# Optimization experiments

Hardware: AMD Instinct MI355X
Metric: run time of the kernel (lower is better)

Reference implementation:

```python
import jax, jax.numpy as jnp
import numpy as np

MAX_IT = 10
LAMBDA_ROF = 4.0
SIGMA = 1.0 / (7.0 * 0.01)
TAU = 0.01
THETA = 0.5
M, N = 2048, 2048


def forward_grad(x):
    """x: [1,M,N] -> [2,M,N]; forward differences, zero at last col/row."""
    gh = jnp.pad(x[0, :, 1:] - x[0, :, :-1], ((0, 0), (0, 1)))  # horizontal
    gv = jnp.pad(x[0, 1:, :] - x[0, :-1, :], ((0, 1), (0, 0)))  # vertical
    return jnp.stack([gh, gv], axis=0)


def backward_div(y):
    """y: [2,M,N] -> [1,M,N]; adjoint backward-difference divergence."""
    yh, yv = y[0], y[1]
    d_h = jnp.concatenate([yh[:, :1], yh[:, 1:-1] - yh[:, :-2], -yh[:, -2:-1]], axis=1)
    d_v = jnp.concatenate([yv[:1, :], yv[1:-1, :] - yv[:-2, :], -yv[-2:-1, :]], axis=0)
    return (d_h + d_v)[None]  # [1,M,N]


def prox_linf_ball(p, r):
    # Torch original builds m1/m2 from p.data (no grad flow) -> stop_gradient.
    m1 = jnp.maximum(p - r, 0.0)
    m2 = jnp.maximum(-p - r, 0.0)
    return p - jax.lax.stop_gradient(m1 - m2)  # == clamp(p, -r, r) in value


def setup_inputs() -> dict:
    key = jax.random.key(0)
    k1, k2 = jax.random.split(key)
    img_obs = jax.random.uniform(k1, (1, M, N), dtype=jnp.float32)
    w1 = jnp.array([0.5], dtype=jnp.float32)  # nn.Parameter [1]
    w2 = jnp.array([0.4], dtype=jnp.float32)  # nn.Parameter [1]
    return {"img_obs": img_obs, "w1": w1, "w2": w2}


def reference(img_obs, w1, w2):
    x = img_obs
    x_tilde = img_obs
    y = forward_grad(x)  # [2,M,N]
    # w_term built from y.data in torch -> constant wrt autodiff
    w_term = jax.lax.stop_gradient(jnp.exp(-jnp.abs(y)))
    w = w1[0] + w2[0] * w_term  # [2,M,N]
    for _ in range(MAX_IT):
        # dual weighted update + L-inf prox
        y = y + SIGMA * w * forward_grad(x_tilde)
        y = prox_linf_ball(y, 1.0)
        # primal weighted update (ROF)
        x_old = x
        x = (x + TAU * backward_div(w * y) + LAMBDA_ROF * TAU * img_obs) / (1.0 + LAMBDA_ROF * TAU)
        # primal over-relaxation
        x_tilde = x + THETA * (x - x_old)
    return x_tilde
```

## Files before the change

### kernel.cpp

```cpp
#include <hip/hip_runtime.h>


namespace {
constexpr int M = 2048, N = 2048;
constexpr float SIGMA     = 1.0f / (7.0f * 0.01f);
constexpr float TAU       = 0.01f;
constexpr float TAUIS     = TAU * (7.0f * 0.01f);
constexpr float LT        = 4.0f * 0.01f;
constexpr float INV_DEN   = 1.0f / (1.0f + 4.0f * 0.01f);
constexpr int TW = 64, TH = 48;
constexpr int PC = 88;
constexpr int PR = 68;
constexpr int UPR = 22;
constexpr int PROC = 67;
constexpr int NU = PROC * UPR;
constexpr int NT = 512;
constexpr int NPASS = 3;
constexpr int GY = (M + TH - 1) / TH;
}

typedef _Float16 h4 __attribute__((ext_vector_type(4)));

__device__ inline h4 h4splat(float v) {
    _Float16 s = (_Float16)v;
    return (h4){s, s, s, s};
}
__device__ inline int imax(int a, int b) { return a > b ? a : b; }

__global__ __launch_bounds__(NT, 4) void pd_fused(
    const float* __restrict__ img, float* __restrict__ out,
    const float* __restrict__ w1p, const float* __restrict__ w2p)
{
    __shared__ __align__(16) float    sXT[PR * PC];
    __shared__ __align__(16) _Float16 sQV[PR * PC];
    __shared__ __align__(16) _Float16 sQH3[1536];

    const int tid  = threadIdx.x;
    const int lane = tid & 63;
    const int c0 = blockIdx.x * TW, r0 = blockIdx.y * TH;
    const int gr0 = r0 - 10, gc0 = c0 - 12;
    const float w1 = w1p[0], w2 = w2p[0];

    int bF_[NPASS], dth_[NPASS];
    #pragma unroll
    for (int p = 0; p < NPASS; ++p) {
        int u = tid + p * NT;
        int li = u / UPR, uj = u - li * UPR;
        int lc = uj * 4;
        bF_[p] = u * 4;
        int d = imax(imax(9 - li, li - (TH + 9)), imax(8 - lc, lc - 75));
        d = imax(d, 0);
        if (u >= NU) d = 100;
        dth_[p] = d;
    }

    #pragma unroll
    for (int p = 0; p < NPASS; ++p) {
        int su = tid + p * NT;
        if (su < PR * UPR) {
            int li = su / UPR, uj = su - li * UPR;
            int gi = gr0 + li, gj = gc0 + uj * 4;
            float4 v = make_float4(0.f, 0.f, 0.f, 0.f);
            if ((unsigned)gi < (unsigned)M && (unsigned)gj <= (unsigned)(N - 4))
                v = *(const float4*)&img[(size_t)gi * N + gj];
            *(float4*)&sXT[su * 4] = v;
        }
    }
    __syncthreads();

    float xr[NPASS][4], xt[NPASS][4];
    h4 xi[NPASS], yh[NPASS], yv[NPASS], swh[NPASS], swv[NPASS], qH[NPASS];

    #pragma unroll
    for (int p = 0; p < NPASS; ++p) {
        int u = tid + p * NT, bF = bF_[p];
        float4 c = make_float4(0.f, 0.f, 0.f, 0.f);
        if (u < NU) c = *(const float4*)&sXT[bF];
        float rr = __shfl_down(c.x, 1, 64);
        if (u < NU) {
            int li = u / UPR;
            int gi = gr0 + li, gjb = gc0 + (u - li * UPR) * 4;
            if (lane == 63) rr = sXT[bF + 4];
            float4 dn = *(const float4*)&sXT[bF + PC];
            float ca[4] = {c.x, c.y, c.z, c.w};
            float da[4] = {dn.x, dn.y, dn.z, dn.w};
            bool rok = (unsigned)gi < (unsigned)M;
            bool vok = rok && (gi < M - 1);
            h4 qv;
            #pragma unroll
            for (int l = 0; l < 4; ++l) {
                int gj = gjb + l;
                bool cok = (unsigned)gj < (unsigned)N;
                bool hok = rok && cok && (gj < N - 1);
                bool vk  = vok && cok;
                float nxt = (l < 3) ? ca[l + 1] : rr;
                float gh = hok ? nxt - ca[l] : 0.f;
                float gv = vk  ? da[l] - ca[l] : 0.f;
                float wh = fmaf(w2, __expf(-fabsf(gh)), w1);
                float wv = fmaf(w2, __expf(-fabsf(gv)), w1);
                float y0h = fminf(fmaxf(gh * fmaf(SIGMA, wh, 1.f), -1.f), 1.f);
                float y0v = fminf(fmaxf(gv * fmaf(SIGMA, wv, 1.f), -1.f), 1.f);
                float sh = hok ? SIGMA * wh : 0.f;
                float sv = vk  ? SIGMA * wv : 0.f;
                yh[p][l]  = (_Float16)y0h;  yv[p][l]  = (_Float16)y0v;
                swh[p][l] = (_Float16)sh;   swv[p][l] = (_Float16)sv;
                qH[p][l]  = (_Float16)(sh * y0h);
                qv[l]     = (_Float16)(sv * y0v);
                xr[p][l] = ca[l]; xt[p][l] = ca[l];
                xi[p][l] = (_Float16)ca[l];
            }
            *(h4*)&sQV[bF] = qv;
            sQH3[u] = qH[p][3];
        }
    }
    __syncthreads();

    auto dual = [&](int rem) {
        #pragma unroll
        for (int p = 0; p < NPASS; ++p) {
            float rr = __shfl_down(xt[p][0], 1, 64);
            if (rem >= dth_[p]) {
                int bF = bF_[p];
                if (lane == 63) rr = sXT[bF + 4];
                float4 dn = *(const float4*)&sXT[bF + PC];
                float da[4] = {dn.x, dn.y, dn.z, dn.w};
                h4 ghh, gvh;
                #pragma unroll
                for (int l = 0; l < 4; ++l) {
                    float nxt = (l < 3) ? xt[p][l + 1] : rr;
                    ghh[l] = (_Float16)(nxt - xt[p][l]);
                    gvh[l] = (_Float16)(da[l] - xt[p][l]);
                }
                h4 nh = yh[p] + swh[p] * ghh;
                h4 nv = yv[p] + swv[p] * gvh;
                nh = __builtin_elementwise_min(__builtin_elementwise_max(nh, h4splat(-1.f)), h4splat(1.f));
                nv = __builtin_elementwise_min(__builtin_elementwise_max(nv, h4splat(-1.f)), h4splat(1.f));
                yh[p] = nh; yv[p] = nv;
                h4 qh = swh[p] * nh;
                h4 qv = swv[p] * nv;
                qH[p] = qh;
                *(h4*)&sQV[bF] = qv;
                sQH3[bF >> 2] = qh[3];
            }
        }
    };

    auto primal = [&](int rem) {
        #pragma unroll
        for (int p = 0; p < NPASS; ++p) {
            if (rem >= dth_[p]) {
                int bF = bF_[p];
                int bu = (bF >= UPR * 4) ? bF - PC : bF;
                h4 qvu = *(const h4*)&sQV[bu];
                h4 qv  = *(const h4*)&sQV[bF];
                _Float16 qhl = sQH3[imax((bF >> 2) - 1, 0)];
                h4 qsh;
                qsh[0] = qhl; qsh[1] = qH[p][0]; qsh[2] = qH[p][1]; qsh[3] = qH[p][2];
                h4 dvg = (qH[p] - qsh) + (qv - qvu);
                float xtv[4];
                #pragma unroll
                for (int l = 0; l < 4; ++l) {
                    float dv = (float)dvg[l];
                    float xo = xr[p][l];
                    float xn = (fmaf(TAUIS, dv, xo) + LT * (float)xi[p][l]) * INV_DEN;
                    xr[p][l] = xn;
                    float v = fmaf(0.5f, xn - xo, xn);
                    xt[p][l] = v; xtv[l] = v;
                }
                *(float4*)&sXT[bF] = make_float4(xtv[0], xtv[1], xtv[2], xtv[3]);
            }
        }
    };

    primal(9);
    __syncthreads();
    #pragma unroll 1
    for (int t = 1; t < 10; ++t) {
        int rem = 9 - t;
        dual(rem);
        __syncthreads();
        primal(rem);
        __syncthreads();
    }

    #pragma unroll
    for (int v = tid; v < TH * (TW / 4); v += NT) {
        int row = v >> 4;
        int cu  = v & 15;
        int gi = r0 + row;
        if (gi < M) {
            float4 o = *(const float4*)&sXT[(10 + row) * PC + 12 + 4 * cu];
            *(float4*)&out[(size_t)gi * N + (c0 + 4 * cu)] = o;
        }
    }
}

extern "C" void kernel_launch(void* const* d_in, const int* in_sizes, int n_in,
                              void* d_out, int out_size, void* d_ws, size_t ws_size,
                              hipStream_t stream)
{
    const float* img = (const float*)d_in[0];
    const float* w1  = (const float*)d_in[1];
    const float* w2  = (const float*)d_in[2];
    float* out = (float*)d_out;

    dim3 grid(N / TW, GY);
    pd_fused<<<grid, NT, 0, stream>>>(img, out, w1, w2);
}
```

Before: 121.9 us.

## Store over-relaxed primal tile in fp16 shared memory and write output directly

```diff
diff --git a/kernel.cpp b/kernel.cpp
--- a/kernel.cpp
+++ b/kernel.cpp
@@ -4,8 +4,7 @@
 namespace {
 constexpr int M = 2048, N = 2048;
 constexpr float SIGMA     = 1.0f / (7.0f * 0.01f);
-constexpr float TAU       = 0.01f;
-constexpr float TAUIS     = TAU * (7.0f * 0.01f);
+constexpr float TAUIS     = 0.01f * (7.0f * 0.01f);
 constexpr float LT        = 4.0f * 0.01f;
 constexpr float INV_DEN   = 1.0f / (1.0f + 4.0f * 0.01f);
 constexpr int TW = 64, TH = 48;
@@ -20,18 +19,26 @@
 }
 
 typedef _Float16 h4 __attribute__((ext_vector_type(4)));
+typedef unsigned uint32;
 
 __device__ inline h4 h4splat(float v) {
     _Float16 s = (_Float16)v;
     return (h4){s, s, s, s};
 }
 __device__ inline int imax(int a, int b) { return a > b ? a : b; }
+__device__ inline uint32 abit(uint32 hi, uint32 lo) {
+    return __builtin_amdgcn_alignbit(hi, lo, 16);
+}
+__device__ inline h4 clamp1(h4 v) {
+    return __builtin_elementwise_min(
+               __builtin_elementwise_max(v, h4splat(-1.f)), h4splat(1.f));
+}
 
 __global__ __launch_bounds__(NT, 4) void pd_fused(
     const float* __restrict__ img, float* __restrict__ out,
     const float* __restrict__ w1p, const float* __restrict__ w2p)
 {
-    __shared__ __align__(16) float    sXT[PR * PC];
+    __shared__ __align__(16) _Float16 sXT16[PR * PC];
     __shared__ __align__(16) _Float16 sQV[PR * PC];
     __shared__ __align__(16) _Float16 sQH3[1536];
 
@@ -41,13 +48,11 @@
     const int gr0 = r0 - 10, gc0 = c0 - 12;
     const float w1 = w1p[0], w2 = w2p[0];
 
-    int bF_[NPASS], dth_[NPASS];
+    int dth_[NPASS];
     #pragma unroll
     for (int p = 0; p < NPASS; ++p) {
         int u = tid + p * NT;
-        int li = u / UPR, uj = u - li * UPR;
-        int lc = uj * 4;
-        bF_[p] = u * 4;
+        int li = u / UPR, lc = (u - li * UPR) * 4;
         int d = imax(imax(9 - li, li - (TH + 9)), imax(8 - lc, lc - 75));
         d = imax(d, 0);
         if (u >= NU) d = 100;
@@ -63,27 +68,30 @@
             float4 v = make_float4(0.f, 0.f, 0.f, 0.f);
             if ((unsigned)gi < (unsigned)M && (unsigned)gj <= (unsigned)(N - 4))
                 v = *(const float4*)&img[(size_t)gi * N + gj];
-            *(float4*)&sXT[su * 4] = v;
+            h4 h; h[0] = (_Float16)v.x; h[1] = (_Float16)v.y;
+                  h[2] = (_Float16)v.z; h[3] = (_Float16)v.w;
+            *(h4*)&sXT16[su * 4] = h;
         }
     }
     __syncthreads();
 
-    float xr[NPASS][4], xt[NPASS][4];
-    h4 xi[NPASS], yh[NPASS], yv[NPASS], swh[NPASS], swv[NPASS], qH[NPASS];
+    float xr[NPASS][4];
+    h4 xt16[NPASS], xi16[NPASS], yh[NPASS], yv[NPASS],
+       swh[NPASS], swv[NPASS], qH[NPASS];
 
     #pragma unroll
     for (int p = 0; p < NPASS; ++p) {
-        int u = tid + p * NT, bF = bF_[p];
-        float4 c = make_float4(0.f, 0.f, 0.f, 0.f);
-        if (u < NU) c = *(const float4*)&sXT[bF];
-        float rr = __shfl_down(c.x, 1, 64);
+        int u = tid + p * NT;
         if (u < NU) {
+            int bF = u * 4;
             int li = u / UPR;
             int gi = gr0 + li, gjb = gc0 + (u - li * UPR) * 4;
-            if (lane == 63) rr = sXT[bF + 4];
-            float4 dn = *(const float4*)&sXT[bF + PC];
-            float ca[4] = {c.x, c.y, c.z, c.w};
-            float da[4] = {dn.x, dn.y, dn.z, dn.w};
+            h4 c16 = *(const h4*)&sXT16[bF];
+            uint32 rrp = *(const uint32*)&sXT16[bF + 4];
+            h4 dn = *(const h4*)&sXT16[bF + PC];
+            uint2 xu = __builtin_bit_cast(uint2, c16);
+            h4 xsh = __builtin_bit_cast(h4,
+                         make_uint2(abit(xu.y, xu.x), abit(rrp, xu.y)));
             bool rok = (unsigned)gi < (unsigned)M;
             bool vok = rok && (gi < M - 1);
             h4 qv;
@@ -93,22 +101,21 @@
                 bool cok = (unsigned)gj < (unsigned)N;
                 bool hok = rok && cok && (gj < N - 1);
                 bool vk  = vok && cok;
-                float nxt = (l < 3) ? ca[l + 1] : rr;
-                float gh = hok ? nxt - ca[l] : 0.f;
-                float gv = vk  ? da[l] - ca[l] : 0.f;
-                float wh = fmaf(w2, __expf(-fabsf(gh)), w1);
-                float wv = fmaf(w2, __expf(-fabsf(gv)), w1);
-                float y0h = fminf(fmaxf(gh * fmaf(SIGMA, wh, 1.f), -1.f), 1.f);
-                float y0v = fminf(fmaxf(gv * fmaf(SIGMA, wv, 1.f), -1.f), 1.f);
+                float ghf = hok ? (float)xsh[l] - (float)c16[l] : 0.f;
+                float gvf = vk  ? (float)dn[l]  - (float)c16[l] : 0.f;
+                float wh = fmaf(w2, __expf(-fabsf(ghf)), w1);
+                float wv = fmaf(w2, __expf(-fabsf(gvf)), w1);
+                float y0h = fminf(fmaxf(ghf * fmaf(SIGMA, wh, 1.f), -1.f), 1.f);
+                float y0v = fminf(fmaxf(gvf * fmaf(SIGMA, wv, 1.f), -1.f), 1.f);
                 float sh = hok ? SIGMA * wh : 0.f;
                 float sv = vk  ? SIGMA * wv : 0.f;
                 yh[p][l]  = (_Float16)y0h;  yv[p][l]  = (_Float16)y0v;
                 swh[p][l] = (_Float16)sh;   swv[p][l] = (_Float16)sv;
                 qH[p][l]  = (_Float16)(sh * y0h);
                 qv[l]     = (_Float16)(sv * y0v);
-                xr[p][l] = ca[l]; xt[p][l] = ca[l];
-                xi[p][l] = (_Float16)ca[l];
+                xr[p][l]  = (float)c16[l];
             }
+            xi16[p] = c16; xt16[p] = c16;
             *(h4*)&sQV[bF] = qv;
             sQH3[u] = qH[p][3];
         }
@@ -118,23 +125,18 @@
     auto dual = [&](int rem) {
         #pragma unroll
         for (int p = 0; p < NPASS; ++p) {
-            float rr = __shfl_down(xt[p][0], 1, 64);
+            uint2 xu = __builtin_bit_cast(uint2, xt16[p]);
+            uint32 rrp = __shfl_down(xu.x, 1, 64);
             if (rem >= dth_[p]) {
-                int bF = bF_[p];
-                if (lane == 63) rr = sXT[bF + 4];
-                float4 dn = *(const float4*)&sXT[bF + PC];
-                float da[4] = {dn.x, dn.y, dn.z, dn.w};
-                h4 ghh, gvh;
-                #pragma unroll
-                for (int l = 0; l < 4; ++l) {
-                    float nxt = (l < 3) ? xt[p][l + 1] : rr;
-                    ghh[l] = (_Float16)(nxt - xt[p][l]);
-                    gvh[l] = (_Float16)(da[l] - xt[p][l]);
-                }
-                h4 nh = yh[p] + swh[p] * ghh;
-                h4 nv = yv[p] + swv[p] * gvh;
-                nh = __builtin_elementwise_min(__builtin_elementwise_max(nh, h4splat(-1.f)), h4splat(1.f));
-                nv = __builtin_elementwise_min(__builtin_elementwise_max(nv, h4splat(-1.f)), h4splat(1.f));
+                int bF = (tid + p * NT) * 4;
+                if (lane == 63) rrp = *(const uint32*)&sXT16[bF + 4];
+                h4 dn = *(const h4*)&sXT16[bF + PC];
+                h4 xsh = __builtin_bit_cast(h4,
+                             make_uint2(abit(xu.y, xu.x), abit(rrp, xu.y)));
+                h4 ghh = xsh - xt16[p];
+                h4 gvh = dn  - xt16[p];
+                h4 nh = clamp1(yh[p] + swh[p] * ghh);
+                h4 nv = clamp1(yv[p] + swv[p] * gvh);
                 yh[p] = nh; yv[p] = nv;
                 h4 qh = swh[p] * nh;
                 h4 qv = swv[p] * nv;
@@ -145,53 +147,54 @@
         }
     };
 
-    auto primal = [&](int rem) {
+    auto primal = [&](int rem, bool last) {
         #pragma unroll
         for (int p = 0; p < NPASS; ++p) {
             if (rem >= dth_[p]) {
-                int bF = bF_[p];
+                int u = tid + p * NT, bF = u * 4;
                 int bu = (bF >= UPR * 4) ? bF - PC : bF;
                 h4 qvu = *(const h4*)&sQV[bu];
                 h4 qv  = *(const h4*)&sQV[bF];
-                _Float16 qhl = sQH3[imax((bF >> 2) - 1, 0)];
-                h4 qsh;
-                qsh[0] = qhl; qsh[1] = qH[p][0]; qsh[2] = qH[p][1]; qsh[3] = qH[p][2];
+                uint32 qhl = *(const unsigned short*)&sQH3[imax(u - 1, 0)];
+                uint2 qu = __builtin_bit_cast(uint2, qH[p]);
+                h4 qsh = __builtin_bit_cast(h4,
+                             make_uint2(abit(qu.x, qhl << 16), abit(qu.y, qu.x)));
                 h4 dvg = (qH[p] - qsh) + (qv - qvu);
                 float xtv[4];
                 #pragma unroll
                 for (int l = 0; l < 4; ++l) {
                     float dv = (float)dvg[l];
                     float xo = xr[p][l];
-                    float xn = (fmaf(TAUIS, dv, xo) + LT * (float)xi[p][l]) * INV_DEN;
+                    float xn = (fmaf(TAUIS, dv, xo) + LT * (float)xi16[p][l]) * INV_DEN;
                     xr[p][l] = xn;
-                    float v = fmaf(0.5f, xn - xo, xn);
-                    xt[p][l] = v; xtv[l] = v;
+                    xtv[l] = fmaf(0.5f, xn - xo, xn);
                 }
-                *(float4*)&sXT[bF] = make_float4(xtv[0], xtv[1], xtv[2], xtv[3]);
+                if (!last) {
+                    h4 nx; nx[0] = (_Float16)xtv[0]; nx[1] = (_Float16)xtv[1];
+                           nx[2] = (_Float16)xtv[2]; nx[3] = (_Float16)xtv[3];
+                    xt16[p] = nx;
+                    *(h4*)&sXT16[bF] = nx;
+                } else {
+                    int li = u / UPR, uj = u - li * UPR;
+                    int gi = gr0 + li;
+                    if (li >= 10 && uj >= 3 && uj <= 18 && gi < M) {
+                        *(float4*)&out[(size_t)gi * N + (gc0 + uj * 4)] =
+                            make_float4(xtv[0], xtv[1], xtv[2], xtv[3]);
+                    }
+                }
             }
         }
     };
 
-    primal(9);
+    primal(9, false);
     __syncthreads();
     #pragma unroll 1
     for (int t = 1; t < 10; ++t) {
         int rem = 9 - t;
         dual(rem);
         __syncthreads();
-        primal(rem);
+        primal(rem, t == 9);
         __syncthreads();
-    }
-
-    #pragma unroll
-    for (int v = tid; v < TH * (TW / 4); v += NT) {
-        int row = v >> 4;
-        int cu  = v & 15;
-        int gi = r0 + row;
-        if (gi < M) {
-            float4 o = *(const float4*)&sXT[(10 + row) * PC + 12 + 4 * cu];
-            *(float4*)&out[(size_t)gi * N + (c0 + 4 * cu)] = o;
-        }
     }
 }
 
```

Result: faster. 116.9 us (-4.1%).
